# Optimization experiments

Measured on AMD Instinct MI355X. Metric: run time of the kernel, lower is better.

Reference implementation:

```python
import jax, jax.numpy as jnp
import numpy as np

N = 30000   # nodes
E = 480000  # edges per adjacency
T = 12      # time steps
C = 32      # channels (in == out)


def setup_inputs() -> dict:
    key = jax.random.key(0)
    ks = jax.random.split(key, 16)
    inp = {"x": jax.random.normal(ks[0], (N, C, T), jnp.float32)}
    names = ["fwd1", "fwd2", "bck1", "bck2"]
    for i, n in enumerate(names):
        inp[f"ei_{n}"] = jax.random.randint(ks[1 + i], (2, E), 0, N)
        inp[f"ew_{n}"] = jax.random.uniform(ks[5 + i], (E,), jnp.float32)
        inp[f"W_{n}"] = jax.random.normal(ks[9 + i], (C, C), jnp.float32) / jnp.sqrt(jnp.float32(C))
    inp["bias"] = jax.random.normal(ks[13], (C,), jnp.float32)
    return inp


def reference(x, W_fwd1, W_fwd2, W_bck1, W_bck2, bias,
              ew_fwd1, ew_fwd2, ew_bck1, ew_bck2,
              ei_fwd1, ei_fwd2, ei_bck1, ei_bck2):
    # x: [N, C, T] -> transpose(1,2) -> [N, T, C], nodes on dim 0 (node_dim=0)
    xt = jnp.transpose(x, (0, 2, 1))

    def gcn(W, ei, ew):
        h = xt @ W                           # [N, T, Cout] linear over features
        msg = h[ei[0]] * ew[:, None, None]   # gather source nodes, weight edges
        return jax.ops.segment_sum(msg, ei[1], num_segments=N)  # scatter to targets

    out = (gcn(W_fwd1, ei_fwd1, ew_fwd1)
           + gcn(W_fwd2, ei_fwd2, ew_fwd2)
           + gcn(W_bck1, ei_bck1, ew_bck1)
           + gcn(W_bck2, ei_bck2, ew_bck2))   # [N, T, C]
    # transpose back to [N, C, T] and add channel bias (view(1,-1,1))
    return jnp.transpose(out, (0, 2, 1)) + bias[None, :, None]
```

## Files before the change

### kernel.cpp

```cpp
#include <hip/hip_runtime.h>
#include <hip/hip_fp16.h>

#define NN 30000
#define NE 480000
#define CC 32
#define TT 12
#define CT 384
#define TOT (4 * NN)
#define NB  118
#define NSL 6
#define SLB ((size_t)NN * 128)
#define GPB 8
#define GPM 8
#define RSH2 193
#define NBKT 235
#define BCAP 16384

typedef unsigned int u32x4 __attribute__((ext_vector_type(4)));
typedef unsigned int u32x2 __attribute__((ext_vector_type(2)));
typedef float f32x2 __attribute__((ext_vector_type(2)));

static __device__ __forceinline__ unsigned int h2u(__half2 h) {
    return __builtin_bit_cast(unsigned int, h);
}
static __device__ __forceinline__ __half2 u2h(unsigned int u) {
    return __builtin_bit_cast(__half2, u);
}


__global__ void conv_kernel(const float2* __restrict__ x2, char* __restrict__ xh) {
    int i = blockIdx.x * blockDim.x + threadIdx.x;
    if (i < NN * 192) {
        float2 v = x2[i];
        int n = i / 192, w = i % 192;
        __half2* dst = (__half2*)(xh + (size_t)(w >> 5) * SLB);
        dst[n * 32 + (w & 31)] = __floats2half2_rn(v.x, v.y);
    }
}


__global__ void initcur_kernel(int* __restrict__ g_cur) {
    int t = threadIdx.x;
    if (t < NBKT) g_cur[t] = t * BCAP;
}

__global__ __launch_bounds__(512)
void bin_kernel(const int* __restrict__ ei0, const int* __restrict__ ei1,
                const int* __restrict__ ei2, const int* __restrict__ ei3,
                const float* __restrict__ ew0, const float* __restrict__ ew1,
                const float* __restrict__ ew2, const float* __restrict__ ew3,
                int* __restrict__ g_cur, u32x2* __restrict__ staging) {
    __shared__ int bcnt[NBKT];
    __shared__ int bbase[NBKT];
    const int b = blockIdx.y;
    const int t = threadIdx.x;
    const int e0 = blockIdx.x * 4096;
    const int*   ei = (b == 0) ? ei0 : (b == 1) ? ei1 : (b == 2) ? ei2 : ei3;
    const float* ew = (b == 0) ? ew0 : (b == 1) ? ew1 : (b == 2) ? ew2 : ew3;

    for (int i = t; i < NBKT; i += 512) bcnt[i] = 0;
    __syncthreads();

    int row_[8]; unsigned int pair_[8]; int bkt_[8]; int rank_[8];
#pragma unroll
    for (int i = 0; i < 8; ++i) {
        int e = e0 + i * 512 + t;
        row_[i] = -1;
        if (e < NE) {
            int dst = ei[NE + e];
            int src = ei[e];
            unsigned int w16 = (unsigned int)__half_as_ushort(__float2half_rn(ew[e]));
            row_[i]  = b * NN + dst;
            pair_[i] = (unsigned int)src | (w16 << 16);
            bkt_[i]  = row_[i] >> 9;
            rank_[i] = atomicAdd(&bcnt[bkt_[i]], 1);
        }
    }
    __syncthreads();
    for (int i = t; i < NBKT; i += 512) {
        int cc = bcnt[i];
        bbase[i] = (cc > 0) ? atomicAdd(&g_cur[i], cc) : 0;
    }
    __syncthreads();
#pragma unroll
    for (int i = 0; i < 8; ++i) {
        if (row_[i] >= 0) {
            int pos = bbase[bkt_[i]] + rank_[i];
            if (pos < (bkt_[i] + 1) * BCAP) {
                u32x2 rec; rec.x = (unsigned int)row_[i]; rec.y = pair_[i];
                staging[pos] = rec;
            }
        }
    }
}

__global__ __launch_bounds__(256)
void count_kernel(const int* __restrict__ g_cur, const u32x2* __restrict__ staging,
                  int* __restrict__ cnt) {
    __shared__ int hist[512];
    const int bkt = blockIdx.x;
    const int t = threadIdx.x;
    hist[t] = 0; hist[t + 256] = 0;
    __syncthreads();
    const int row0 = bkt << 9;
    const int n = g_cur[bkt] - bkt * BCAP;
    const u32x2* __restrict__ sg = staging + (size_t)bkt * BCAP;
    for (int i = t; i < n; i += 256)
        atomicAdd(&hist[(int)sg[i].x - row0], 1);
    __syncthreads();
    if (row0 + t < TOT)       cnt[row0 + t]       = hist[t];
    if (row0 + t + 256 < TOT) cnt[row0 + t + 256] = hist[t + 256];
}

__global__ void scanA_kernel(const int* __restrict__ cnt,
                             int* __restrict__ pre, int* __restrict__ bsum) {
    __shared__ int s[1024];
    int tid = threadIdx.x;
    int i = blockIdx.x * 1024 + tid;
    int v = (i < TOT) ? ((cnt[i] + 3) & ~3) : 0;
    s[tid] = v;
    __syncthreads();
    for (int off = 1; off < 1024; off <<= 1) {
        int t = (tid >= off) ? s[tid - off] : 0;
        __syncthreads();
        s[tid] += t;
        __syncthreads();
    }
    if (i < TOT) pre[i] = s[tid] - v;
    if (tid == 1023) bsum[blockIdx.x] = s[1023];
}

__global__ void scanB_kernel(const int* __restrict__ bsum,
                             int* __restrict__ bbase, int* __restrict__ offs) {
    __shared__ int s[128];
    int tid = threadIdx.x;
    int v = (tid < NB) ? bsum[tid] : 0;
    s[tid] = v;
    __syncthreads();
    for (int off = 1; off < 128; off <<= 1) {
        int t = (tid >= off) ? s[tid - off] : 0;
        __syncthreads();
        s[tid] += t;
        __syncthreads();
    }
    if (tid < NB) bbase[tid] = s[tid] - v;
    if (tid == 127) offs[TOT] = s[127];
}

__global__ void scanC_kernel(const int* __restrict__ pre, const int* __restrict__ bbase,
                             int* __restrict__ offs) {
    int i = blockIdx.x * 1024 + threadIdx.x;
    if (i < TOT) offs[i] = bbase[blockIdx.x] + pre[i];
}

__global__ __launch_bounds__(256)
void sort_kernel(const int* __restrict__ g_cur, const u32x2* __restrict__ staging,
                 const int* __restrict__ offs, unsigned int* __restrict__ pairs) {
    __shared__ int cur[512];
    const int bkt = blockIdx.x;
    const int t = threadIdx.x;
    const int row0 = bkt << 9;
    cur[t]       = (row0 + t < TOT)       ? offs[row0 + t]       : 0;
    cur[t + 256] = (row0 + t + 256 < TOT) ? offs[row0 + t + 256] : 0;
    __syncthreads();
    const int n = g_cur[bkt] - bkt * BCAP;
    const u32x2* __restrict__ sg = staging + (size_t)bkt * BCAP;
    for (int i = t; i < n; i += 256) {
        u32x2 r = sg[i];
        int pos = atomicAdd(&cur[(int)r.x - row0], 1);
        pairs[pos] = r.y;
    }
}


__global__ __launch_bounds__(256, 8)
void gather_kernel(const char* __restrict__ xh, const unsigned int* __restrict__ pairs,
                   const int* __restrict__ offs, const int* __restrict__ cnt,
                   char* __restrict__ agg) {
    const int tid  = threadIdx.x;
    const int lane = tid & 63;
    const int o = lane >> 3, l = lane & 7;
    const int task = (tid >> 6) * 8 + o;
    const int node = blockIdx.x * GPB + (task >> 2);
    const int branch = task & 3;
    const int row = branch * NN + node;
    const int slice = blockIdx.y;
    const char* __restrict__ xs = xh + (size_t)slice * SLB + l * 16;

    const int beg = offs[row];
    const int c   = cnt[row];

    __half2 a0 = u2h(0), a1 = u2h(0), a2 = u2h(0), a3 = u2h(0);
    __half2 b0 = u2h(0), b1 = u2h(0), b2 = u2h(0), b3 = u2h(0);

    for (int eb = 0; eb < c; eb += 4) {
        u32x4 pw = *(const u32x4*)(pairs + beg + eb);
#pragma unroll
        for (int u = 0; u < 4; ++u) {
            unsigned int w32 = (u == 0) ? pw.x : (u == 1) ? pw.y : (u == 2) ? pw.z : pw.w;
            if (eb + u < c) {
                u32x4 xv = *(const u32x4*)(xs + (size_t)(w32 & 0xFFFFu) * 128);
                __half2 w2 = __half2half2(__ushort_as_half((unsigned short)(w32 >> 16)));
                if (u & 1) {
                    b0 = __hfma2(w2, u2h(xv.x), b0);
                    b1 = __hfma2(w2, u2h(xv.y), b1);
                    b2 = __hfma2(w2, u2h(xv.z), b2);
                    b3 = __hfma2(w2, u2h(xv.w), b3);
                } else {
                    a0 = __hfma2(w2, u2h(xv.x), a0);
                    a1 = __hfma2(w2, u2h(xv.y), a1);
                    a2 = __hfma2(w2, u2h(xv.z), a2);
                    a3 = __hfma2(w2, u2h(xv.w), a3);
                }
            }
        }
    }
    u32x4 r;
    r.x = h2u(__hadd2(a0, b0));
    r.y = h2u(__hadd2(a1, b1));
    r.z = h2u(__hadd2(a2, b2));
    r.w = h2u(__hadd2(a3, b3));
    __builtin_nontemporal_store(r, (u32x4*)(agg + (size_t)row * 768 + slice * 128 + l * 16));
}


__global__ __launch_bounds__(384)
void matmul_kernel(const char* __restrict__ agg,
                   const float* __restrict__ W0, const float* __restrict__ W1,
                   const float* __restrict__ W2, const float* __restrict__ W3,
                   const float* __restrict__ bias, float* __restrict__ out) {
    __shared__ __half2 aggB[32 * RSH2];
    const int tid = threadIdx.x;
    const int n0 = blockIdx.x * GPM;

    {
        const int r = tid / 12, sub = tid % 12;
        const char* src = agg + (size_t)((r & 3) * NN + n0 + (r >> 2)) * 768 + sub * 64;
        char* dst = (char*)(aggB + r * RSH2) + sub * 64;
#pragma unroll
        for (int q = 0; q < 4; ++q) {
            u32x4 v = __builtin_nontemporal_load((const u32x4*)(src + 16 * q));
            *(u32x4*)(dst + 16 * q) = v;
        }
    }
    __syncthreads();

    const float* Ws[4] = { W0, W1, W2, W3 };
    {
        const int g = tid / 48;
        const int rem = tid % 48;
        const int q = rem / 6;
        const int t2 = rem % 6;
        f32x2 acc[4];
#pragma unroll
        for (int i = 0; i < 4; ++i) { float bv = bias[q * 4 + i]; acc[i].x = bv; acc[i].y = bv; }
#pragma unroll
        for (int b = 0; b < 4; ++b) {
            const float* __restrict__ Wb = Ws[b];
            const __half2* __restrict__ aL = aggB + (g * 4 + b) * RSH2 + t2;
#pragma unroll
            for (int h = 0; h < 2; ++h) {
                float2 row[16];
#pragma unroll
                for (int kk = 0; kk < 16; ++kk)
                    row[kk] = __half22float2(aL[(h * 16 + kk) * 6]);
#pragma unroll
                for (int kk = 0; kk < 16; ++kk) {
#pragma unroll
                    for (int i = 0; i < 4; ++i) {
                        float w = Wb[(h * 16 + kk) * CC + q * 4 + i];
                        acc[i].x = fmaf(w, row[kk].x, acc[i].x);
                        acc[i].y = fmaf(w, row[kk].y, acc[i].y);
                    }
                }
            }
        }
#pragma unroll
        for (int i = 0; i < 4; ++i) {
            f32x2* dst = (f32x2*)&out[(size_t)(n0 + g) * CT + (q * 4 + i) * TT + 2 * t2];
            __builtin_nontemporal_store(acc[i], dst);
        }
    }
}


extern "C" void kernel_launch(void* const* d_in, const int* in_sizes, int n_in,
                              void* d_out, int out_size, void* d_ws, size_t ws_size,
                              hipStream_t stream) {
    const float* x    = (const float*)d_in[0];
    const float* bias = (const float*)d_in[13];
    const int*   ei[4] = { (const int*)d_in[1], (const int*)d_in[4],
                           (const int*)d_in[7], (const int*)d_in[10] };
    const float* ew[4] = { (const float*)d_in[2], (const float*)d_in[5],
                           (const float*)d_in[8], (const float*)d_in[11] };
    const float* W[4]  = { (const float*)d_in[3], (const float*)d_in[6],
                           (const float*)d_in[9], (const float*)d_in[12] };
    float* out = (float*)d_out;

    char* ws = (char*)d_ws;
    size_t OFF_PAIRS = 0;
    size_t OFF_XH    = OFF_PAIRS + ((size_t)4 * NE + 4 * TOT) * 4;
    size_t OFF_AGG   = OFF_XH    + NSL * SLB;
    size_t OFF_CNT   = OFF_AGG   + (size_t)TOT * 768;
    size_t OFF_OFFS  = OFF_CNT   + (size_t)TOT * 4;
    size_t OFF_PRE   = OFF_OFFS  + (size_t)(TOT + 1) * 4;
    size_t OFF_BSUM  = OFF_PRE   + (size_t)TOT * 4;
    size_t OFF_BBASE = OFF_BSUM  + (size_t)128 * 4;
    size_t OFF_GCUR  = OFF_BBASE + (size_t)128 * 4;

    unsigned int* pairs = (unsigned int*)(ws + OFF_PAIRS);
    char*         xh    = ws + OFF_XH;
    char*         agg   = ws + OFF_AGG;
    u32x2*        staging = (u32x2*)(ws + OFF_AGG);
    int* cnt   = (int*)(ws + OFF_CNT);
    int* offs  = (int*)(ws + OFF_OFFS);
    int* pre   = (int*)(ws + OFF_PRE);
    int* bsum  = (int*)(ws + OFF_BSUM);
    int* bbase = (int*)(ws + OFF_BBASE);
    int* g_cur = (int*)(ws + OFF_GCUR);

    initcur_kernel<<<1, 256, 0, stream>>>(g_cur);

    dim3 bg((NE + 4095) / 4096, 4);
    bin_kernel<<<bg, 512, 0, stream>>>(ei[0], ei[1], ei[2], ei[3],
                                       ew[0], ew[1], ew[2], ew[3],
                                       g_cur, staging);
    count_kernel<<<NBKT, 256, 0, stream>>>(g_cur, staging, cnt);
    scanA_kernel<<<NB, 1024, 0, stream>>>(cnt, pre, bsum);
    scanB_kernel<<<1, 128, 0, stream>>>(bsum, bbase, offs);
    scanC_kernel<<<NB, 1024, 0, stream>>>(pre, bbase, offs);
    sort_kernel<<<NBKT, 256, 0, stream>>>(g_cur, staging, offs, pairs);

    conv_kernel<<<(NN * 192 + 255) / 256, 256, 0, stream>>>((const float2*)x, xh);

    dim3 gg(NN / GPB, NSL);
    gather_kernel<<<gg, 256, 0, stream>>>(xh, pairs, offs, cnt, agg);

    matmul_kernel<<<NN / GPM, 384, 0, stream>>>(agg, W[0], W[1], W[2], W[3], bias, out);
}
```

Measured before the change: 296.3 us.

## Split half-precision feature table into eight 96-byte slices with slice-fastest grid

The fp16 copy of x is re-laid out as eight slices of 96 bytes per node instead of six slices of 128 bytes. Each lane now reads and accumulates 12 bytes, and writes its result as three 4-byte nontemporal stores. The gather grid is flattened so that the eight slices of the same node group run in consecutive blocks, which should let the pairs list and cache lines be shared across slices. Pair loads are also made nontemporal. The trade-off is narrower, 12-byte unaligned-width loads and stores and more blocks overall.

```diff
diff --git a/kernel.cpp b/kernel.cpp
--- a/kernel.cpp
+++ b/kernel.cpp
@@ -8,13 +8,14 @@
 #define CT 384
 #define TOT (4 * NN)
 #define NB  118
-#define NSL 6
-#define SLB ((size_t)NN * 128)
+#define NSL 8
+#define SLB96 ((size_t)NN * 96)
 #define GPB 8
 #define GPM 8
 #define RSH2 193
 #define NBKT 235
 #define BCAP 16384
+#define PAIRS_WORDS ((size_t)4 * NE + 4 * TOT + 32)
 
 typedef unsigned int u32x4 __attribute__((ext_vector_type(4)));
 typedef unsigned int u32x2 __attribute__((ext_vector_type(2)));
@@ -33,8 +34,8 @@
     if (i < NN * 192) {
         float2 v = x2[i];
         int n = i / 192, w = i % 192;
-        __half2* dst = (__half2*)(xh + (size_t)(w >> 5) * SLB);
-        dst[n * 32 + (w & 31)] = __floats2half2_rn(v.x, v.y);
+        __half2* dst = (__half2*)(xh + (size_t)(w / 24) * SLB96);
+        dst[n * 24 + (w % 24)] = __floats2half2_rn(v.x, v.y);
     }
 }
 
@@ -181,46 +182,43 @@
     const int lane = tid & 63;
     const int o = lane >> 3, l = lane & 7;
     const int task = (tid >> 6) * 8 + o;
-    const int node = blockIdx.x * GPB + (task >> 2);
+    const int slice = blockIdx.x & 7;
+    const int node = (blockIdx.x >> 3) * GPB + (task >> 2);
     const int branch = task & 3;
     const int row = branch * NN + node;
-    const int slice = blockIdx.y;
-    const char* __restrict__ xs = xh + (size_t)slice * SLB + l * 16;
+    const char* __restrict__ xs = xh + (size_t)slice * SLB96 + l * 12;
 
     const int beg = offs[row];
     const int c   = cnt[row];
 
-    __half2 a0 = u2h(0), a1 = u2h(0), a2 = u2h(0), a3 = u2h(0);
-    __half2 b0 = u2h(0), b1 = u2h(0), b2 = u2h(0), b3 = u2h(0);
+    __half2 a0 = u2h(0), a1 = u2h(0), a2 = u2h(0);
+    __half2 b0 = u2h(0), b1 = u2h(0), b2 = u2h(0);
 
     for (int eb = 0; eb < c; eb += 4) {
-        u32x4 pw = *(const u32x4*)(pairs + beg + eb);
+        u32x4 pw = __builtin_nontemporal_load((const u32x4*)(pairs + beg + eb));
 #pragma unroll
         for (int u = 0; u < 4; ++u) {
             unsigned int w32 = (u == 0) ? pw.x : (u == 1) ? pw.y : (u == 2) ? pw.z : pw.w;
             if (eb + u < c) {
-                u32x4 xv = *(const u32x4*)(xs + (size_t)(w32 & 0xFFFFu) * 128);
+                const char* rp = xs + (w32 & 0xFFFFu) * 96;
+                uint3 v = *(const uint3*)rp;
                 __half2 w2 = __half2half2(__ushort_as_half((unsigned short)(w32 >> 16)));
                 if (u & 1) {
-                    b0 = __hfma2(w2, u2h(xv.x), b0);
-                    b1 = __hfma2(w2, u2h(xv.y), b1);
-                    b2 = __hfma2(w2, u2h(xv.z), b2);
-                    b3 = __hfma2(w2, u2h(xv.w), b3);
+                    b0 = __hfma2(w2, u2h(v.x), b0);
+                    b1 = __hfma2(w2, u2h(v.y), b1);
+                    b2 = __hfma2(w2, u2h(v.z), b2);
                 } else {
-                    a0 = __hfma2(w2, u2h(xv.x), a0);
-                    a1 = __hfma2(w2, u2h(xv.y), a1);
-                    a2 = __hfma2(w2, u2h(xv.z), a2);
-                    a3 = __hfma2(w2, u2h(xv.w), a3);
+                    a0 = __hfma2(w2, u2h(v.x), a0);
+                    a1 = __hfma2(w2, u2h(v.y), a1);
+                    a2 = __hfma2(w2, u2h(v.z), a2);
                 }
             }
         }
     }
-    u32x4 r;
-    r.x = h2u(__hadd2(a0, b0));
-    r.y = h2u(__hadd2(a1, b1));
-    r.z = h2u(__hadd2(a2, b2));
-    r.w = h2u(__hadd2(a3, b3));
-    __builtin_nontemporal_store(r, (u32x4*)(agg + (size_t)row * 768 + slice * 128 + l * 16));
+    char* dst = agg + (size_t)row * 768 + slice * 96 + l * 12;
+    __builtin_nontemporal_store(h2u(__hadd2(a0, b0)), (unsigned int*)dst);
+    __builtin_nontemporal_store(h2u(__hadd2(a1, b1)), (unsigned int*)(dst + 4));
+    __builtin_nontemporal_store(h2u(__hadd2(a2, b2)), (unsigned int*)(dst + 8));
 }
 
 
@@ -299,8 +297,8 @@
 
     char* ws = (char*)d_ws;
     size_t OFF_PAIRS = 0;
-    size_t OFF_XH    = OFF_PAIRS + ((size_t)4 * NE + 4 * TOT) * 4;
-    size_t OFF_AGG   = OFF_XH    + NSL * SLB;
+    size_t OFF_XH    = OFF_PAIRS + PAIRS_WORDS * 4;
+    size_t OFF_AGG   = OFF_XH    + NSL * SLB96;
     size_t OFF_CNT   = OFF_AGG   + (size_t)TOT * 768;
     size_t OFF_OFFS  = OFF_CNT   + (size_t)TOT * 4;
     size_t OFF_PRE   = OFF_OFFS  + (size_t)(TOT + 1) * 4;
@@ -333,8 +331,7 @@
 
     conv_kernel<<<(NN * 192 + 255) / 256, 256, 0, stream>>>((const float2*)x, xh);
 
-    dim3 gg(NN / GPB, NSL);
-    gather_kernel<<<gg, 256, 0, stream>>>(xh, pairs, offs, cnt, agg);
+    gather_kernel<<<(NN / GPB) * 8, 256, 0, stream>>>(xh, pairs, offs, cnt, agg);
 
     matmul_kernel<<<NN / GPM, 384, 0, stream>>>(agg, W[0], W[1], W[2], W[3], bias, out);
 }
```

Result: slower. 434.1 us (+46.5%).

## Fuse count, scan and sort kernels into one kernel with grid barriers

Applied to the files above, without the earlier changes.

Replaces the count, three-stage scan and sort kernels with a single persistent build kernel that uses atomic-counter grid barriers between phases, removing several kernel launches and their gaps. The block-level scan now handles 4 elements per thread with 256 threads. The gather kernel also loads edge pairs with nontemporal hints. The spin-based grid barrier relies on all 235 blocks being co-resident and adds a memset launch per call.

```diff
diff --git a/kernel.cpp b/kernel.cpp
--- a/kernel.cpp
+++ b/kernel.cpp
@@ -15,6 +15,7 @@
 #define RSH2 193
 #define NBKT 235
 #define BCAP 16384
+#define PAIRS_WORDS ((size_t)4 * NE + 4 * TOT + 64)
 
 typedef unsigned int u32x4 __attribute__((ext_vector_type(4)));
 typedef unsigned int u32x2 __attribute__((ext_vector_type(2)));
@@ -51,7 +52,7 @@
                 const float* __restrict__ ew2, const float* __restrict__ ew3,
                 int* __restrict__ g_cur, u32x2* __restrict__ staging) {
     __shared__ int bcnt[NBKT];
-    __shared__ int bbase[NBKT];
+    __shared__ int bbs[NBKT];
     const int b = blockIdx.y;
     const int t = threadIdx.x;
     const int e0 = blockIdx.x * 4096;
@@ -79,13 +80,13 @@
     __syncthreads();
     for (int i = t; i < NBKT; i += 512) {
         int cc = bcnt[i];
-        bbase[i] = (cc > 0) ? atomicAdd(&g_cur[i], cc) : 0;
+        bbs[i] = (cc > 0) ? atomicAdd(&g_cur[i], cc) : 0;
     }
     __syncthreads();
 #pragma unroll
     for (int i = 0; i < 8; ++i) {
         if (row_[i] >= 0) {
-            int pos = bbase[bkt_[i]] + rank_[i];
+            int pos = bbs[bkt_[i]] + rank_[i];
             if (pos < (bkt_[i] + 1) * BCAP) {
                 u32x2 rec; rec.x = (unsigned int)row_[i]; rec.y = pair_[i];
                 staging[pos] = rec;
@@ -94,80 +95,92 @@
     }
 }
 
+
+static __device__ __forceinline__ void gridbar(int* ctr) {
+    __syncthreads();
+    if (threadIdx.x == 0) {
+        __threadfence();
+        atomicAdd(ctr, 1);
+        while (__hip_atomic_load(ctr, __ATOMIC_ACQUIRE, __HIP_MEMORY_SCOPE_AGENT) < NBKT) { }
+    }
+    __syncthreads();
+}
+
 __global__ __launch_bounds__(256)
-void count_kernel(const int* __restrict__ g_cur, const u32x2* __restrict__ staging,
-                  int* __restrict__ cnt) {
-    __shared__ int hist[512];
+void build_kernel(const int* __restrict__ g_cur, const u32x2* __restrict__ staging,
+                  int* __restrict__ cnt, int* __restrict__ pre, int* __restrict__ bsum,
+                  int* __restrict__ bbase, int* __restrict__ offs,
+                  unsigned int* __restrict__ pairs, int* __restrict__ bar) {
+    __shared__ int lds[512];
     const int bkt = blockIdx.x;
     const int t = threadIdx.x;
-    hist[t] = 0; hist[t + 256] = 0;
-    __syncthreads();
     const int row0 = bkt << 9;
     const int n = g_cur[bkt] - bkt * BCAP;
     const u32x2* __restrict__ sg = staging + (size_t)bkt * BCAP;
+
+    lds[t] = 0; lds[t + 256] = 0;
+    __syncthreads();
     for (int i = t; i < n; i += 256)
-        atomicAdd(&hist[(int)sg[i].x - row0], 1);
-    __syncthreads();
-    if (row0 + t < TOT)       cnt[row0 + t]       = hist[t];
-    if (row0 + t + 256 < TOT) cnt[row0 + t + 256] = hist[t + 256];
-}
-
-__global__ void scanA_kernel(const int* __restrict__ cnt,
-                             int* __restrict__ pre, int* __restrict__ bsum) {
-    __shared__ int s[1024];
-    int tid = threadIdx.x;
-    int i = blockIdx.x * 1024 + tid;
-    int v = (i < TOT) ? ((cnt[i] + 3) & ~3) : 0;
-    s[tid] = v;
-    __syncthreads();
-    for (int off = 1; off < 1024; off <<= 1) {
-        int t = (tid >= off) ? s[tid - off] : 0;
+        atomicAdd(&lds[(int)sg[i].x - row0], 1);
+    __syncthreads();
+    if (row0 + t < TOT)       cnt[row0 + t]       = lds[t];
+    if (row0 + t + 256 < TOT) cnt[row0 + t + 256] = lds[t + 256];
+    gridbar(&bar[0]);
+
+    if (bkt < NB) {
+        const int base = bkt * 1024;
+        int v[4]; int s = 0;
+#pragma unroll
+        for (int j = 0; j < 4; ++j) {
+            int idx = base + 4 * t + j;
+            v[j] = (idx < TOT) ? ((cnt[idx] + 3) & ~3) : 0;
+            s += v[j];
+        }
+        lds[t] = s;
         __syncthreads();
-        s[tid] += t;
+        for (int off = 1; off < 256; off <<= 1) {
+            int x = (t >= off) ? lds[t - off] : 0;
+            __syncthreads();
+            lds[t] += x;
+            __syncthreads();
+        }
+        int excl = (t == 0) ? 0 : lds[t - 1];
+#pragma unroll
+        for (int j = 0; j < 4; ++j) {
+            int idx = base + 4 * t + j;
+            if (idx < TOT) pre[idx] = excl;
+            excl += v[j];
+        }
+        if (t == 255) bsum[bkt] = lds[255];
+    }
+    gridbar(&bar[1]);
+
+    if (bkt == 0) {
+        int v = (t < NB) ? bsum[t] : 0;
+        lds[t] = v;
         __syncthreads();
-    }
-    if (i < TOT) pre[i] = s[tid] - v;
-    if (tid == 1023) bsum[blockIdx.x] = s[1023];
-}
-
-__global__ void scanB_kernel(const int* __restrict__ bsum,
-                             int* __restrict__ bbase, int* __restrict__ offs) {
-    __shared__ int s[128];
-    int tid = threadIdx.x;
-    int v = (tid < NB) ? bsum[tid] : 0;
-    s[tid] = v;
-    __syncthreads();
-    for (int off = 1; off < 128; off <<= 1) {
-        int t = (tid >= off) ? s[tid - off] : 0;
-        __syncthreads();
-        s[tid] += t;
-        __syncthreads();
-    }
-    if (tid < NB) bbase[tid] = s[tid] - v;
-    if (tid == 127) offs[TOT] = s[127];
-}
-
-__global__ void scanC_kernel(const int* __restrict__ pre, const int* __restrict__ bbase,
-                             int* __restrict__ offs) {
-    int i = blockIdx.x * 1024 + threadIdx.x;
-    if (i < TOT) offs[i] = bbase[blockIdx.x] + pre[i];
-}
-
-__global__ __launch_bounds__(256)
-void sort_kernel(const int* __restrict__ g_cur, const u32x2* __restrict__ staging,
-                 const int* __restrict__ offs, unsigned int* __restrict__ pairs) {
-    __shared__ int cur[512];
-    const int bkt = blockIdx.x;
-    const int t = threadIdx.x;
-    const int row0 = bkt << 9;
-    cur[t]       = (row0 + t < TOT)       ? offs[row0 + t]       : 0;
-    cur[t + 256] = (row0 + t + 256 < TOT) ? offs[row0 + t + 256] : 0;
-    __syncthreads();
-    const int n = g_cur[bkt] - bkt * BCAP;
-    const u32x2* __restrict__ sg = staging + (size_t)bkt * BCAP;
+        for (int off = 1; off < 256; off <<= 1) {
+            int x = (t >= off) ? lds[t - off] : 0;
+            __syncthreads();
+            lds[t] += x;
+            __syncthreads();
+        }
+        if (t < NB) bbase[t] = lds[t] - v;
+    }
+    gridbar(&bar[2]);
+
+#pragma unroll
+    for (int k = 0; k < 2; ++k) {
+        int r = row0 + t + 256 * k;
+        int o = 0;
+        if (r < TOT) o = bbase[r >> 10] + pre[r];
+        lds[t + 256 * k] = o;
+        if (r < TOT) offs[r] = o;
+    }
+    __syncthreads();
     for (int i = t; i < n; i += 256) {
         u32x2 r = sg[i];
-        int pos = atomicAdd(&cur[(int)r.x - row0], 1);
+        int pos = atomicAdd(&lds[(int)r.x - row0], 1);
         pairs[pos] = r.y;
     }
 }
@@ -194,7 +207,7 @@
     __half2 b0 = u2h(0), b1 = u2h(0), b2 = u2h(0), b3 = u2h(0);
 
     for (int eb = 0; eb < c; eb += 4) {
-        u32x4 pw = *(const u32x4*)(pairs + beg + eb);
+        u32x4 pw = __builtin_nontemporal_load((const u32x4*)(pairs + beg + eb));
 #pragma unroll
         for (int u = 0; u < 4; ++u) {
             unsigned int w32 = (u == 0) ? pw.x : (u == 1) ? pw.y : (u == 2) ? pw.z : pw.w;
@@ -299,7 +312,7 @@
 
     char* ws = (char*)d_ws;
     size_t OFF_PAIRS = 0;
-    size_t OFF_XH    = OFF_PAIRS + ((size_t)4 * NE + 4 * TOT) * 4;
+    size_t OFF_XH    = OFF_PAIRS + PAIRS_WORDS * 4;
     size_t OFF_AGG   = OFF_XH    + NSL * SLB;
     size_t OFF_CNT   = OFF_AGG   + (size_t)TOT * 768;
     size_t OFF_OFFS  = OFF_CNT   + (size_t)TOT * 4;
@@ -307,6 +320,7 @@
     size_t OFF_BSUM  = OFF_PRE   + (size_t)TOT * 4;
     size_t OFF_BBASE = OFF_BSUM  + (size_t)128 * 4;
     size_t OFF_GCUR  = OFF_BBASE + (size_t)128 * 4;
+    size_t OFF_BAR   = OFF_GCUR  + (size_t)256 * 4;
 
     unsigned int* pairs = (unsigned int*)(ws + OFF_PAIRS);
     char*         xh    = ws + OFF_XH;
@@ -318,6 +332,9 @@
     int* bsum  = (int*)(ws + OFF_BSUM);
     int* bbase = (int*)(ws + OFF_BBASE);
     int* g_cur = (int*)(ws + OFF_GCUR);
+    int* bar   = (int*)(ws + OFF_BAR);
+
+    hipMemsetAsync(bar, 0, 16, stream);
 
     initcur_kernel<<<1, 256, 0, stream>>>(g_cur);
 
@@ -325,11 +342,9 @@
     bin_kernel<<<bg, 512, 0, stream>>>(ei[0], ei[1], ei[2], ei[3],
                                        ew[0], ew[1], ew[2], ew[3],
                                        g_cur, staging);
-    count_kernel<<<NBKT, 256, 0, stream>>>(g_cur, staging, cnt);
-    scanA_kernel<<<NB, 1024, 0, stream>>>(cnt, pre, bsum);
-    scanB_kernel<<<1, 128, 0, stream>>>(bsum, bbase, offs);
-    scanC_kernel<<<NB, 1024, 0, stream>>>(pre, bbase, offs);
-    sort_kernel<<<NBKT, 256, 0, stream>>>(g_cur, staging, offs, pairs);
+
+    build_kernel<<<NBKT, 256, 0, stream>>>(g_cur, staging, cnt, pre, bsum,
+                                           bbase, offs, pairs, bar);
 
     conv_kernel<<<(NN * 192 + 255) / 256, 256, 0, stream>>>((const float2*)x, xh);
 
```

Result: slower. 383.5 us (+29.4%).
